# Kernel optimization log

Hardware: AMD Instinct MI355X
Metric: run time of the kernel (lower is better)

Reference implementation:

```python
import math
import jax, jax.numpy as jnp
import numpy as np

T_MIN = 0.1
T_MAX = 1.0


def _log_cond_prob(energy, text_mask, mel_mask, direction, neg):
    # energy: (B, I, J); returns (B, I, J, K) with K=J (alpha) or J-1 (beta)
    B, I, J = energy.shape
    if direction == 'alpha':
        K = J
        tri_jk = jnp.arange(J)[:, None] >= jnp.arange(K)[None, :]  # torch triu: valid if j >= k
    else:
        K = J - 1
        tri_jk = jnp.arange(J)[:, None] <= jnp.arange(K)[None, :]  # torch tril: valid if j <= k
    tm = text_mask[:, :, None, None]           # (B,I,1,1)
    mmj = mel_mask[:, None, :, None]           # (B,1,J,1)
    mmk = mel_mask[:, None, None, :K]          # (B,1,1,K)
    mask = tm & mmj & mmk                      # (B,I,J,K)
    tri = tri_jk[None, None] & mask
    mask_invalid = jnp.broadcast_to(tm & mmk, (B, I, J, K))
    text_invalid = jnp.broadcast_to(tm, (B, I, J, K))
    right_mask = mask | (~mask_invalid)
    e = jnp.broadcast_to(energy[..., None], (B, I, J, K))
    e = jnp.where((~tri) & mask_invalid, neg, e)
    e = jnp.where(~mask_invalid, -10.0, e)
    e = e - jax.nn.logsumexp(e, axis=2, keepdims=True)  # normalize over mel dim j
    e = jnp.where(~mask_invalid, neg, e)
    e = jnp.where(~right_mask, -10.0, e)
    e = jnp.where(~text_invalid, -10.0, e)
    return e


def _roll(x, shifts, axis):
    # per-batch roll of x along `axis` by shifts[b]
    return jax.vmap(lambda xb, s: jnp.roll(xb, s, axis=axis - 1))(x, shifts)


def _right_shift(x, sh_t, sh_m):
    x = _roll(x, sh_t, 1)
    x = _roll(x, sh_m, 2)
    return _roll(x, sh_m.at[1:].add(-1), 3)  # faithful to in-place shifts_mel_dim[1:] -= 1


def _left_shift(x, sh_t, sh_m):
    x = x[..., None]
    x = _roll(x, -sh_t, 1)
    x = _roll(x, -sh_m, 2)
    return x[..., 0]


def _compute_alpha(lcp_a, neg):
    # alpha[:, i, j] = lse_k(alpha[:, i-1, k] + lcp_a[:, i-1, j-1, k]) for j >= i
    B, I, J, _ = lcp_a.shape
    j_idx = jnp.arange(J + 1)
    row0 = jnp.full((B, J + 1), neg, dtype=lcp_a.dtype).at[:, 0].set(0.0)

    def step(prev, xs):  # prev = alpha[:, i-1, :J]
        lcp_i, i = xs
        new = jax.nn.logsumexp(prev[:, None, :] + lcp_i, axis=2)  # (B, J), index j-1
        row = jnp.concatenate([jnp.full((B, 1), neg, dtype=new.dtype), new], axis=1)
        row = jnp.where(j_idx[None, :] >= i, row, neg)
        return row[:, :J], row

    _, rows = jax.lax.scan(step, row0[:, :J], (jnp.swapaxes(lcp_a, 0, 1), jnp.arange(1, I + 1)))
    return jnp.concatenate([row0[:, None, :], jnp.swapaxes(rows, 0, 1)], axis=1)  # (B, I+1, J+1)


def _compute_beta(lcp_b, neg):
    # beta[:, i, j] = lse_k(beta[:, i+1, k+1] + lcp_b[:, i, j, k]) for j < J+i-I+1
    B, I, J, _ = lcp_b.shape
    j_idx = jnp.arange(J)
    last = jnp.full((B, J), neg, dtype=lcp_b.dtype).at[:, J - 1].set(0.0)

    def step(nxt, xs):
        lcp_i, i = xs
        full = jax.nn.logsumexp(nxt[:, 1:][:, None, :] + lcp_i, axis=2)  # (B, J)
        row = jnp.where(j_idx[None, :] < (J + i - I + 1), full, neg)
        return row, row

    _, rows = jax.lax.scan(step, last, (jnp.swapaxes(lcp_b[:, :I - 1], 0, 1), jnp.arange(I - 1)), reverse=True)
    return jnp.concatenate([jnp.swapaxes(rows, 0, 1), last[:, None, :]], axis=1)  # (B, I, J)


def _forward(text_embeddings, mel_embeddings, text_mask, mel_mask, noise, temperature_ratio, neg):
    B, I, Dt = text_embeddings.shape
    _, J, Dm = mel_embeddings.shape
    energy = jnp.einsum('bid,bjd->bij', text_embeddings, mel_embeddings) / math.sqrt(Dt * Dm)
    temp = T_MIN + (T_MAX - T_MIN) * temperature_ratio[0]
    energy = (energy - jnp.log(-jnp.log(noise))) / temp  # Gumbel noise + temperature
    lcp_a = _log_cond_prob(energy, text_mask, mel_mask, 'alpha', neg)
    alpha = _compute_alpha(lcp_a, neg)
    t_len = text_mask.sum(1)
    m_len = mel_mask.sum(1)
    sh_t = t_len.max() - t_len
    sh_m = m_len.max() - m_len
    lcp_b = _log_cond_prob(energy, text_mask, mel_mask, 'beta', neg)
    lcp_b = _right_shift(lcp_b, sh_t, sh_m)
    beta = _compute_beta(lcp_b, neg)
    beta = _left_shift(beta, sh_t, sh_m)
    gamma = alpha[:, 1:, 1:] + beta
    gamma_mask = text_mask[:, :, None] & mel_mask[:, None, :]
    gls_mask = jnp.broadcast_to(text_mask[:, :, None], (B, I, J)) | gamma_mask
    gamma = jnp.where(gls_mask, gamma, neg)
    gamma = gamma - jax.nn.logsumexp(gamma, axis=1, keepdims=True)  # normalize over text dim
    gamma = jnp.where(gamma_mask, gamma, neg)
    expanded = jnp.einsum('bij,bid->bjd', jnp.exp(gamma), text_embeddings)
    expanded = expanded * mel_mask[:, :, None]
    return gamma, expanded


def setup_inputs() -> dict:
    key = jax.random.key(0)
    k1, k2, k3, k4 = jax.random.split(key, 4)
    B, I, J, Dt, Dm = 1, 128, 640, 256, 256
    text_embeddings = jax.random.normal(k1, (B, I, Dt), dtype=jnp.float32)
    mel_embeddings = jax.random.normal(k2, (B, J, Dm), dtype=jnp.float32)
    text_mask = jnp.ones((B, I), dtype=bool)
    mel_mask = jnp.ones((B, J), dtype=bool)
    noise = jnp.clip(jax.random.uniform(k3, (B, I, J), dtype=jnp.float32), 1e-8, 1.0 - 1e-8)
    temperature_ratio = jax.random.uniform(k4, (1,), dtype=jnp.float32)
    return {
        'text_embeddings': text_embeddings,
        'mel_embeddings': mel_embeddings,
        'text_mask': text_mask,
        'mel_mask': mel_mask,
        'noise': noise,
        'temperature_ratio': temperature_ratio,
    }


def reference(text_embeddings, mel_embeddings, text_mask, mel_mask, noise, temperature_ratio):
    return _forward(text_embeddings, mel_embeddings, text_mask, mel_mask, noise, temperature_ratio, -jnp.inf)
```

## Files before the change

kernel.cpp:

```cpp
#include <hip/hip_runtime.h>
#include <math.h>

constexpr int TI = 128;
constexpr int TJ = 640;
constexpr int TD = 256;
constexpr int EPL = 10;
constexpr int NS  = 3;
constexpr int CH  = 4;
constexpr int NP  = 12;

#define NEG (-1e30f)
#define LOG2E 1.44269504088896340736f
#define LN2   0.69314718055994530942f

__device__ __forceinline__ float rexp2(float x) { return __builtin_amdgcn_exp2f(x); }
__device__ __forceinline__ float rlog2(float x) { return __builtin_amdgcn_logf(x); }

struct MS { float m, s; };
__device__ __forceinline__ MS ms_combine(MS a, MS b) {
    float d = b.m - a.m;
    bool al = d <= 0.0f;
    float m = al ? a.m : b.m;
    float t = rexp2(al ? d : -d);
    float s = al ? fmaf(b.s, t, a.s) : fmaf(a.s, t, b.s);
    return {m, s};
}
__device__ __forceinline__ MS ms_push(MS run, float x) { return ms_combine(run, {x, 1.0f}); }
__device__ __forceinline__ float ms_final(MS a) {
    return (a.m < -1e29f) ? NEG : a.m + rlog2(a.s);
}

template<int CTRL, int RMASK>
__device__ __forceinline__ float dpp_f(float src, float oldv) {
    int r = __builtin_amdgcn_update_dpp(
        __float_as_int(oldv), __float_as_int(src), CTRL, RMASK, 0xF, false);
    return __int_as_float(r);
}
template<int CTRL, int RMASK>
__device__ __forceinline__ MS dpp_ms(MS v) {
    MS t;
    t.m = dpp_f<CTRL, RMASK>(v.m, NEG);
    t.s = dpp_f<CTRL, RMASK>(v.s, 0.0f);
    return t;
}
__device__ __forceinline__ MS wave_incl_scan_ms(MS v) {
    v = ms_combine(dpp_ms<0x111, 0xF>(v), v);
    v = ms_combine(dpp_ms<0x112, 0xF>(v), v);
    v = ms_combine(dpp_ms<0x114, 0xF>(v), v);
    v = ms_combine(dpp_ms<0x118, 0xF>(v), v);
    v = ms_combine(dpp_ms<0x142, 0xA>(v), v);
    v = ms_combine(dpp_ms<0x143, 0xC>(v), v);
    return v;
}
__device__ __forceinline__ MS wave_excl_from_incl_ms(MS incl) {
    return dpp_ms<0x138, 0xF>(incl);
}
__device__ __forceinline__ float wave_incl_scan_add(float v) {
    v += dpp_f<0x111, 0xF>(v, 0.0f);
    v += dpp_f<0x112, 0xF>(v, 0.0f);
    v += dpp_f<0x114, 0xF>(v, 0.0f);
    v += dpp_f<0x118, 0xF>(v, 0.0f);
    v += dpp_f<0x142, 0xA>(v, 0.0f);
    v += dpp_f<0x143, 0xC>(v, 0.0f);
    return v;
}
__device__ __forceinline__ float wave_incl_scan_max(float v) {
    v = fmaxf(v, dpp_f<0x111, 0xF>(v, NEG));
    v = fmaxf(v, dpp_f<0x112, 0xF>(v, NEG));
    v = fmaxf(v, dpp_f<0x114, 0xF>(v, NEG));
    v = fmaxf(v, dpp_f<0x118, 0xF>(v, NEG));
    v = fmaxf(v, dpp_f<0x142, 0xA>(v, NEG));
    v = fmaxf(v, dpp_f<0x143, 0xC>(v, NEG));
    return v;
}
__device__ __forceinline__ float readlane63(float v) {
    return __int_as_float(__builtin_amdgcn_readlane(__float_as_int(v), 63));
}
__device__ __forceinline__ float readlaneN(float v, int n) {
    return __int_as_float(__builtin_amdgcn_readlane(__float_as_int(v), n));
}

__device__ __forceinline__ void cbar() { asm volatile("" ::: "memory"); }
__device__ __forceinline__ int opaque_zero(int v) {
    int r;
    asm("v_xor_b32 %0, %1, %1" : "=v"(r) : "v"(v));
    return r;
}
__device__ __forceinline__ int pollwait(volatile int* flag, int need) {
    int rv;
    do { rv = *flag; } while (rv < need);
    return rv;
}

__device__ __forceinline__ void load10(float* d, const float* s) {
    const float2* p = (const float2*)s;
    #pragma unroll
    for (int k = 0; k < 5; k++) { float2 v = p[k]; d[2*k] = v.x; d[2*k+1] = v.y; }
}
__device__ __forceinline__ void store10(float* d, const float* v) {
    float2* p = (float2*)d;
    #pragma unroll
    for (int k = 0; k < 5; k++) { float2 t; t.x = v[2*k]; t.y = v[2*k+1]; p[k] = t; }
}

__global__ __launch_bounds__(256) void k_melT(
        const float* __restrict__ mel, float* __restrict__ melT) {
    __shared__ float ldsT[64][65];
    int j0 = blockIdx.x * 64, c0 = blockIdx.y * 64, tid = threadIdx.x;
    int rr = tid >> 4, c4 = tid & 15;
    #pragma unroll
    for (int p = 0; p < 4; p++) {
        int r = p * 16 + rr;
        float4 v = *(const float4*)(mel + (size_t)(j0 + r) * TD + c0 + c4 * 4);
        ldsT[c4 * 4 + 0][r] = v.x;
        ldsT[c4 * 4 + 1][r] = v.y;
        ldsT[c4 * 4 + 2][r] = v.z;
        ldsT[c4 * 4 + 3][r] = v.w;
    }
    __syncthreads();
    int jj = tid & 63, cw = tid >> 6;
    #pragma unroll
    for (int p = 0; p < 16; p++) {
        int cc = p * 4 + cw;
        melT[(size_t)(c0 + cc) * TJ + j0 + jj] = ldsT[cc][jj];
    }
}

__global__ __launch_bounds__(640) void k_energy(
        const float* __restrict__ text, const float* __restrict__ melT,
        const float* __restrict__ noise, const float* __restrict__ trat,
        float* __restrict__ energy, float* __restrict__ Ga,
        float* __restrict__ Gb, float* __restrict__ Cst) {
    __shared__ float trowm[TD], trowc[TD], trowp[TD];
    __shared__ float erowm[TJ], erowc[TJ], erowp[TJ];
    __shared__ float pcur[TJ], scur[TJ];
    __shared__ float wred[2][EPL];
    int i = blockIdx.x, tid = threadIdx.x;
    if (tid < TD) {
        trowc[tid] = text[i * TD + tid];
        trowm[tid] = (i > 0)      ? text[(i - 1) * TD + tid] : 0.0f;
        trowp[tid] = (i < TI - 1) ? text[(i + 1) * TD + tid] : 0.0f;
    }
    __syncthreads();
    float temp = 0.1f + 0.9f * trat[0];
    float sc = LOG2E / temp;
    int j = tid;
    float am = 0.0f, ac = 0.0f, ap = 0.0f;
    #pragma unroll 8
    for (int c = 0; c < TD; c++) {
        float m = melT[(size_t)c * TJ + j];
        am = fmaf(trowm[c], m, am);
        ac = fmaf(trowc[c], m, ac);
        ap = fmaf(trowp[c], m, ap);
    }
    float gm = (i > 0)      ? logf(-logf(noise[(i - 1) * TJ + j])) : 0.0f;
    float gc =                logf(-logf(noise[i * TJ + j]));
    float gp = (i < TI - 1) ? logf(-logf(noise[(i + 1) * TJ + j])) : 0.0f;
    erowm[j] = (am * (1.0f / 256.0f) - gm) * sc;
    float e2 = (ac * (1.0f / 256.0f) - gc) * sc;
    erowc[j] = e2;
    erowp[j] = (ap * (1.0f / 256.0f) - gp) * sc;
    energy[i * TJ + j] = e2;
    __syncthreads();
    if (tid < 64) {
        int l = tid;
        MS loc = {NEG, 0.0f};
        #pragma unroll
        for (int q = 0; q < EPL; q++) loc = ms_push(loc, erowc[l * EPL + q]);
        MS off = wave_excl_from_incl_ms(wave_incl_scan_ms(loc));
        MS run = off;
        #pragma unroll
        for (int q = 0; q < EPL; q++) {
            run = ms_push(run, erowc[l * EPL + q]);
            pcur[l * EPL + q] = ms_final(run);
        }
        loc = {NEG, 0.0f};
        #pragma unroll
        for (int q = 0; q < EPL; q++) loc = ms_push(loc, erowc[TJ - 1 - (l * EPL + q)]);
        off = wave_excl_from_incl_ms(wave_incl_scan_ms(loc));
        run = off;
        #pragma unroll
        for (int q = 0; q < EPL; q++) {
            int idx = TJ - 1 - (l * EPL + q);
            run = ms_push(run, erowc[idx]);
            scur[idx] = ms_final(run);
        }
    }
    __syncthreads();
    float ga, gb;
    if (i == 0) ga = (j == 0) ? -scur[0] : NEG;
    else        ga = (j == 0) ? NEG : erowm[j - 1] - scur[j];
    bool has_b = (i <= TI - 2);
    if (has_b) {
        if (i == TI - 2) gb = (j == 1) ? -pcur[TJ - 2] : NEG;
        else             gb = (j == 0) ? NEG : erowp[TJ - j] - pcur[TJ - 1 - j];
    } else gb = NEG;
    int wv = tid >> 6, l = tid & 63;
    float ma = readlane63(wave_incl_scan_max(ga));
    float mb = readlane63(wave_incl_scan_max(gb));
    if (l == 0) { wred[0][wv] = ma; wred[1][wv] = mb; }
    __syncthreads();
    float Ca = wred[0][0], Cb = wred[1][0];
    #pragma unroll
    for (int k = 1; k < EPL; k++) {
        Ca = fmaxf(Ca, wred[0][k]);
        Cb = fmaxf(Cb, wred[1][k]);
    }
    Ga[i * TJ + j] = rexp2(ga - Ca);
    if (has_b) Gb[i * TJ + j] = rexp2(gb - Cb);
    if (tid == 0) { Cst[i] = Ca; if (has_b) Cst[TI + i] = Cb; }
}

__global__ __launch_bounds__(320, 1) void k_scan(
        const float* __restrict__ energy, const float* __restrict__ Ga,
        const float* __restrict__ Gb, const float* __restrict__ Cst,
        float* __restrict__ a, float* __restrict__ b) {
    __shared__ float Gring[NS][CH][TJ];
    __shared__ float Ppring[NP][TJ + 8];
    __shared__ int ready[NS];
    __shared__ int prow, cdone, ocnt[2];
    const int tid = threadIdx.x, wave = tid >> 6, l = tid & 63;
    const bool is_alpha = (blockIdx.x == 0);
    const int nrows = is_alpha ? TI : TI - 1;
    const int nch = (nrows + CH - 1) / CH;
    if (tid < NS) ready[tid] = 0;
    if (tid == 0) { prow = 0; cdone = 0; ocnt[0] = 0; ocnt[1] = 0; }
    __syncthreads();

    if (wave == 0) {
        float C0, C1;
        if (is_alpha) { C0 = Cst[l]; C1 = Cst[64 + l]; }
        else          { C0 = Cst[128 + l]; C1 = Cst[192 + l]; }
        float Pp[EPL];
        #pragma unroll
        for (int q = 0; q < EPL; q++) Pp[q] = 0.0f;
        float rprev = 0.0f, Lam = 0.0f;
        int seen0 = 0, seen1 = 0;
        for (int c = 0; c < nch; c++) {
            int rv = pollwait(&ready[c % NS], c + 1);
            cbar();
            int tok = opaque_zero(rv);
            float Gr[CH][EPL];
            #pragma unroll
            for (int q = 0; q < CH; q++)
                if (c * CH + q < nrows)
                    load10(Gr[q], &Gring[c % NS][q][l * EPL + tok]);
            #pragma unroll
            for (int s = 0; s < CH; s++) {
                int t = c * CH + s;
                if (t < nrows) {
                    float lp[EPL];
                    if (t == 0) {
                        #pragma unroll
                        for (int q = 0; q < EPL; q++) lp[q] = Gr[0][q];
                    } else {
                        float carry = dpp_f<0x138, 0xF>(Pp[EPL - 1], 0.0f);
                        float rp = rprev;
                        lp[0] = carry * rp * Gr[s][0];
                        #pragma unroll
                        for (int q = 1; q < EPL; q++) lp[q] = Pp[q - 1] * rp * Gr[s][q];
                    }
                    #pragma unroll
                    for (int q = 9; q >= 1; q--) lp[q] += lp[q - 1];
                    #pragma unroll
                    for (int q = 9; q >= 2; q--) lp[q] += lp[q - 2];
                    #pragma unroll
                    for (int q = 9; q >= 4; q--) lp[q] += lp[q - 4];
                    #pragma unroll
                    for (int q = 9; q >= 8; q--) lp[q] += lp[q - 8];
                    float incl = wave_incl_scan_add(lp[EPL - 1]);
                    float excl = dpp_f<0x138, 0xF>(incl, 0.0f);
                    #pragma unroll
                    for (int q = 0; q < EPL; q++) Pp[q] = excl + lp[q];
                    float T = readlane63(incl);
                    int idx2 = is_alpha ? t : (126 - t);
                    float Cc = (idx2 < 64) ? readlaneN(C0, idx2) : readlaneN(C1, idx2 - 64);
                    float basev = Lam + Cc;
                    if (t >= NP) {
                        int tf = t - NP;
                        int need = (tf >> 1) + 1;
                        if (tf & 1) {
                            if (seen1 < need) { seen1 = pollwait(&ocnt[1], need); cbar(); }
                        } else {
                            if (seen0 < need) { seen0 = pollwait(&ocnt[0], need); cbar(); }
                        }
                    }
                    int ps = t % NP;
                    store10(&Ppring[ps][l * EPL], Pp);
                    if (l == 0) Ppring[ps][TJ] = basev;
                    cbar();
                    if (l == 0) *(volatile int*)&prow = t + 1;
                    Lam = basev + rlog2(T);
                    rprev = (T > 0.0f) ? __builtin_amdgcn_rcpf(T) : 0.0f;
                }
            }
            cbar();
            if (l == 0) *(volatile int*)&cdone = c + 1;
        }
    } else if (wave <= 2) {
        const float* Gsrc = is_alpha ? Ga : Gb;
        for (int c = wave - 1; c < nch; c += 2) {
            if (c >= NS) { int dv = pollwait(&cdone, c - NS + 1); cbar(); (void)dv; }
            int slot = c % NS;
            int cnt = nrows - c * CH; if (cnt > CH) cnt = CH;
            int m0 = is_alpha ? c * CH : (TI - 2 - c * CH - (cnt - 1));
            const float4* src = (const float4*)(Gsrc + (size_t)m0 * TJ);
            int total4 = cnt * (TJ / 4);
            #pragma unroll
            for (int it = 0; it < CH * TJ / 4 / 64; it++) {
                int o4 = it * 64 + l;
                if (o4 < total4) {
                    float4 v = src[o4];
                    int ri = o4 / 160, c4 = o4 - ri * 160;
                    int s = is_alpha ? ri : (cnt - 1 - ri);
                    ((float4*)Gring[slot][s])[c4] = v;
                }
            }
            __threadfence_block();
            if (l == 0) *(volatile int*)&ready[slot] = c + 1;
        }
    } else {
        int w = wave - 3;
        if (!is_alpha && w == 0) {
            #pragma unroll
            for (int k = 0; k < EPL; k++) {
                int j = l + 64 * k;
                b[(TI - 1) * TJ + j] = (j == TJ - 1) ? 0.0f : NEG;
            }
        }
        for (int t = w; t < nrows; t += 2) {
            int row = is_alpha ? t : (TI - 2 - t);
            const float* Erow = energy + (size_t)row * TJ;
            float ev[EPL];
            #pragma unroll
            for (int k = 0; k < EPL; k++) ev[k] = Erow[l + 64 * k];
            int rv = pollwait(&prow, t + 1);
            cbar();
            int tok = opaque_zero(rv);
            int ps = t % NP;
            float base = Ppring[ps][TJ + tok];
            float ov[EPL];
            #pragma unroll
            for (int k = 0; k < EPL; k++) {
                int j = l + 64 * k;
                int pj = is_alpha ? j : (TJ - 1 - j);
                ov[k] = ev[k] + rlog2(Ppring[ps][pj + tok]) + base;
            }
            float* dst = (is_alpha ? a : b) + (size_t)row * TJ;
            #pragma unroll
            for (int k = 0; k < EPL; k++) dst[l + 64 * k] = ov[k];
            cbar();
            if (l == 0) *(volatile int*)&ocnt[w] = (t >> 1) + 1;
        }
    }
}

__global__ __launch_bounds__(256) void k_gamma(
        const float* __restrict__ a, const float* __restrict__ b,
        const float* __restrict__ text,
        float* __restrict__ outg, float* __restrict__ oute) {
    __shared__ float w128[4][TI];
    __shared__ float redm[4][2], reds[4][2];
    int j0 = blockIdx.x * 4, tid = threadIdx.x;
    float gg[4];
    if (tid < TI) {
        float4 av4 = *(const float4*)(a + (size_t)tid * TJ + j0);
        float4 bv4 = *(const float4*)(b + (size_t)tid * TJ + j0);
        float avs[4] = {av4.x, av4.y, av4.z, av4.w};
        float bvs[4] = {bv4.x, bv4.y, bv4.z, bv4.w};
        #pragma unroll
        for (int c = 0; c < 4; c++) {
            float av = avs[c], bv = bvs[c];
            gg[c] = (av < -1e29f || bv < -1e29f) ? NEG : av + bv;
            MS v = {gg[c], 1.0f};
            #pragma unroll
            for (int off = 32; off > 0; off >>= 1) {
                float om = __shfl_xor(v.m, off, 64);
                float os = __shfl_xor(v.s, off, 64);
                v = ms_combine(v, {om, os});
            }
            if ((tid & 63) == 0) { redm[c][tid >> 6] = v.m; reds[c][tid >> 6] = v.s; }
        }
    }
    __syncthreads();
    float lse[4];
    #pragma unroll
    for (int c = 0; c < 4; c++)
        lse[c] = ms_final(ms_combine({redm[c][0], reds[c][0]}, {redm[c][1], reds[c][1]}));
    if (tid < TI) {
        float og[4];
        #pragma unroll
        for (int c = 0; c < 4; c++) {
            bool fin = gg[c] > -1e29f;
            og[c] = fin ? (gg[c] - lse[c]) * LN2 : NEG;
            w128[c][tid] = fin ? rexp2(gg[c] - lse[c]) : 0.0f;
        }
        *(float4*)(outg + (size_t)tid * TJ + j0) = make_float4(og[0], og[1], og[2], og[3]);
    }
    __syncthreads();
    float acc0 = 0.0f, acc1 = 0.0f, acc2 = 0.0f, acc3 = 0.0f;
    #pragma unroll 4
    for (int ii = 0; ii < TI; ii++) {
        float tv = text[ii * TD + tid];
        acc0 = fmaf(w128[0][ii], tv, acc0);
        acc1 = fmaf(w128[1][ii], tv, acc1);
        acc2 = fmaf(w128[2][ii], tv, acc2);
        acc3 = fmaf(w128[3][ii], tv, acc3);
    }
    oute[(size_t)(j0 + 0) * TD + tid] = acc0;
    oute[(size_t)(j0 + 1) * TD + tid] = acc1;
    oute[(size_t)(j0 + 2) * TD + tid] = acc2;
    oute[(size_t)(j0 + 3) * TD + tid] = acc3;
}

extern "C" void kernel_launch(void* const* d_in, const int* in_sizes, int n_in,
                              void* d_out, int out_size, void* d_ws, size_t ws_size,
                              hipStream_t stream) {
    const float* text  = (const float*)d_in[0];
    const float* mel   = (const float*)d_in[1];
    const float* noise = (const float*)d_in[4];
    const float* trat  = (const float*)d_in[5];

    float* outg = (float*)d_out;
    float* oute = outg + TI * TJ;

    float* w      = (float*)d_ws;
    float* energy = w;
    float* Ga     = w + 1 * TI * TJ;
    float* Gb     = w + 2 * TI * TJ;
    float* Cst    = Gb + (size_t)(TI - 1) * TJ;
    float* melT   = w + 3 * TI * TJ;
    float* aArr   = w + 3 * TI * TJ;
    float* bArr   = w + 4 * TI * TJ;

    k_melT  <<<dim3(TJ / 64, TD / 64), 256, 0, stream>>>(mel, melT);
    k_energy<<<TI, TJ, 0, stream>>>(text, melT, noise, trat, energy, Ga, Gb, Cst);
    k_scan  <<<2, 320, 0, stream>>>(energy, Ga, Gb, Cst, aArr, bArr);
    k_gamma <<<TJ / 4, 256, 0, stream>>>(aArr, bArr, text, outg, oute);
}
```

Measured before the change: 149.4 us.

## Move alpha/beta log-output epilogue from scan kernel into gamma kernel

The scan kernel no longer has output waves that turn the prefix products into alpha/beta log values through a shared-memory ring with handshake polling. The scan wave now writes raw prefix rows and per-row bases straight to global memory. The gamma kernel rebuilds alpha and beta from energy, the prefix rows and the bases, including the special last beta row. This takes synchronization and consumer-wave work off the serial critical path of the two-block scan. In exchange, gamma does extra log work and reads one more array.

```diff
diff --git a/kernel.cpp b/kernel.cpp
--- a/kernel.cpp
+++ b/kernel.cpp
@@ -7,7 +7,6 @@
 constexpr int EPL = 10;
 constexpr int NS  = 3;
 constexpr int CH  = 4;
-constexpr int NP  = 12;
 
 #define NEG (-1e30f)
 #define LOG2E 1.44269504088896340736f
@@ -211,31 +210,32 @@
     if (tid == 0) { Cst[i] = Ca; if (has_b) Cst[TI + i] = Cb; }
 }
 
-__global__ __launch_bounds__(320, 1) void k_scan(
-        const float* __restrict__ energy, const float* __restrict__ Ga,
-        const float* __restrict__ Gb, const float* __restrict__ Cst,
-        float* __restrict__ a, float* __restrict__ b) {
+__global__ __launch_bounds__(192, 1) void k_scan(
+        const float* __restrict__ Ga, const float* __restrict__ Gb,
+        const float* __restrict__ Cst,
+        float* __restrict__ PpA, float* __restrict__ PpB,
+        float* __restrict__ bvA, float* __restrict__ bvB) {
     __shared__ float Gring[NS][CH][TJ];
-    __shared__ float Ppring[NP][TJ + 8];
     __shared__ int ready[NS];
-    __shared__ int prow, cdone, ocnt[2];
+    __shared__ int cdone;
     const int tid = threadIdx.x, wave = tid >> 6, l = tid & 63;
     const bool is_alpha = (blockIdx.x == 0);
     const int nrows = is_alpha ? TI : TI - 1;
     const int nch = (nrows + CH - 1) / CH;
     if (tid < NS) ready[tid] = 0;
-    if (tid == 0) { prow = 0; cdone = 0; ocnt[0] = 0; ocnt[1] = 0; }
+    if (tid == 0) cdone = 0;
     __syncthreads();
 
     if (wave == 0) {
         float C0, C1;
         if (is_alpha) { C0 = Cst[l]; C1 = Cst[64 + l]; }
         else          { C0 = Cst[128 + l]; C1 = Cst[192 + l]; }
+        float* PpOut = is_alpha ? PpA : PpB;
+        float* bvOut = is_alpha ? bvA : bvB;
         float Pp[EPL];
         #pragma unroll
         for (int q = 0; q < EPL; q++) Pp[q] = 0.0f;
         float rprev = 0.0f, Lam = 0.0f;
-        int seen0 = 0, seen1 = 0;
         for (int c = 0; c < nch; c++) {
             int rv = pollwait(&ready[c % NS], c + 1);
             cbar();
@@ -276,20 +276,8 @@
                     int idx2 = is_alpha ? t : (126 - t);
                     float Cc = (idx2 < 64) ? readlaneN(C0, idx2) : readlaneN(C1, idx2 - 64);
                     float basev = Lam + Cc;
-                    if (t >= NP) {
-                        int tf = t - NP;
-                        int need = (tf >> 1) + 1;
-                        if (tf & 1) {
-                            if (seen1 < need) { seen1 = pollwait(&ocnt[1], need); cbar(); }
-                        } else {
-                            if (seen0 < need) { seen0 = pollwait(&ocnt[0], need); cbar(); }
-                        }
-                    }
-                    int ps = t % NP;
-                    store10(&Ppring[ps][l * EPL], Pp);
-                    if (l == 0) Ppring[ps][TJ] = basev;
-                    cbar();
-                    if (l == 0) *(volatile int*)&prow = t + 1;
+                    store10(PpOut + (size_t)t * TJ + l * EPL, Pp);
+                    if (l == 0) bvOut[t] = basev;
                     Lam = basev + rlog2(T);
                     rprev = (T > 0.0f) ? __builtin_amdgcn_rcpf(T) : 0.0f;
                 }
@@ -297,7 +285,7 @@
             cbar();
             if (l == 0) *(volatile int*)&cdone = c + 1;
         }
-    } else if (wave <= 2) {
+    } else {
         const float* Gsrc = is_alpha ? Ga : Gb;
         for (int c = wave - 1; c < nch; c += 2) {
             if (c >= NS) { int dv = pollwait(&cdone, c - NS + 1); cbar(); (void)dv; }
@@ -319,58 +307,40 @@
             __threadfence_block();
             if (l == 0) *(volatile int*)&ready[slot] = c + 1;
         }
-    } else {
-        int w = wave - 3;
-        if (!is_alpha && w == 0) {
-            #pragma unroll
-            for (int k = 0; k < EPL; k++) {
-                int j = l + 64 * k;
-                b[(TI - 1) * TJ + j] = (j == TJ - 1) ? 0.0f : NEG;
-            }
-        }
-        for (int t = w; t < nrows; t += 2) {
-            int row = is_alpha ? t : (TI - 2 - t);
-            const float* Erow = energy + (size_t)row * TJ;
-            float ev[EPL];
-            #pragma unroll
-            for (int k = 0; k < EPL; k++) ev[k] = Erow[l + 64 * k];
-            int rv = pollwait(&prow, t + 1);
-            cbar();
-            int tok = opaque_zero(rv);
-            int ps = t % NP;
-            float base = Ppring[ps][TJ + tok];
-            float ov[EPL];
-            #pragma unroll
-            for (int k = 0; k < EPL; k++) {
-                int j = l + 64 * k;
-                int pj = is_alpha ? j : (TJ - 1 - j);
-                ov[k] = ev[k] + rlog2(Ppring[ps][pj + tok]) + base;
-            }
-            float* dst = (is_alpha ? a : b) + (size_t)row * TJ;
-            #pragma unroll
-            for (int k = 0; k < EPL; k++) dst[l + 64 * k] = ov[k];
-            cbar();
-            if (l == 0) *(volatile int*)&ocnt[w] = (t >> 1) + 1;
-        }
     }
 }
 
 __global__ __launch_bounds__(256) void k_gamma(
-        const float* __restrict__ a, const float* __restrict__ b,
-        const float* __restrict__ text,
+        const float* __restrict__ E, const float* __restrict__ PpA,
+        const float* __restrict__ PpB, const float* __restrict__ bvA,
+        const float* __restrict__ bvB, const float* __restrict__ text,
         float* __restrict__ outg, float* __restrict__ oute) {
     __shared__ float w128[4][TI];
     __shared__ float redm[4][2], reds[4][2];
     int j0 = blockIdx.x * 4, tid = threadIdx.x;
     float gg[4];
     if (tid < TI) {
-        float4 av4 = *(const float4*)(a + (size_t)tid * TJ + j0);
-        float4 bv4 = *(const float4*)(b + (size_t)tid * TJ + j0);
-        float avs[4] = {av4.x, av4.y, av4.z, av4.w};
-        float bvs[4] = {bv4.x, bv4.y, bv4.z, bv4.w};
+        float4 e4 = *(const float4*)(E + (size_t)tid * TJ + j0);
+        float4 pa4 = *(const float4*)(PpA + (size_t)tid * TJ + j0);
+        float es[4] = {e4.x, e4.y, e4.z, e4.w};
+        float pas[4] = {pa4.x, pa4.y, pa4.z, pa4.w};
+        float bva = bvA[tid];
+        float bvs[4];
+        if (tid == TI - 1) {
+            #pragma unroll
+            for (int c = 0; c < 4; c++) bvs[c] = ((j0 + c) == TJ - 1) ? 0.0f : NEG;
+        } else {
+            int tb = TI - 2 - tid;
+            float4 pb4 = *(const float4*)(PpB + (size_t)tb * TJ + (TJ - 4 - j0));
+            float pbs[4] = {pb4.w, pb4.z, pb4.y, pb4.x};
+            float bvb = bvB[tb];
+            #pragma unroll
+            for (int c = 0; c < 4; c++) bvs[c] = es[c] + rlog2(pbs[c]) + bvb;
+        }
         #pragma unroll
         for (int c = 0; c < 4; c++) {
-            float av = avs[c], bv = bvs[c];
+            float av = es[c] + rlog2(pas[c]) + bva;
+            float bv = bvs[c];
             gg[c] = (av < -1e29f || bv < -1e29f) ? NEG : av + bv;
             MS v = {gg[c], 1.0f};
             #pragma unroll
@@ -429,12 +399,14 @@
     float* Ga     = w + 1 * TI * TJ;
     float* Gb     = w + 2 * TI * TJ;
     float* Cst    = Gb + (size_t)(TI - 1) * TJ;
+    float* bvA    = Cst + 256;
+    float* bvB    = Cst + 384;
     float* melT   = w + 3 * TI * TJ;
-    float* aArr   = w + 3 * TI * TJ;
-    float* bArr   = w + 4 * TI * TJ;
+    float* PpA    = w + 3 * TI * TJ;
+    float* PpB    = w + 4 * TI * TJ;
 
     k_melT  <<<dim3(TJ / 64, TD / 64), 256, 0, stream>>>(mel, melT);
     k_energy<<<TI, TJ, 0, stream>>>(text, melT, noise, trat, energy, Ga, Gb, Cst);
-    k_scan  <<<2, 320, 0, stream>>>(energy, Ga, Gb, Cst, aArr, bArr);
-    k_gamma <<<TJ / 4, 256, 0, stream>>>(aArr, bArr, text, outg, oute);
-}
+    k_scan  <<<2, 192, 0, stream>>>(Ga, Gb, Cst, PpA, PpB, bvA, bvB);
+    k_gamma <<<TJ / 4, 256, 0, stream>>>(energy, PpA, PpB, bvA, bvB, text, outg, oute);
+}
```

After: 148.6 us. No clear change (-0.5%).
